# Kernel optimization log

Hardware: AMD Instinct MI355X
Metric: run time of the kernel (lower is better)

Reference implementation:

```python
import jax, jax.numpy as jnp
import numpy as np

B, CIN, COUT, H, W = 16, 128, 128, 64, 64
K1, K2, DIL = 3, 3, 1
PAD0 = DIL * (K1 - 1) // 2
PAD1 = DIL * (K2 - 1) // 2
L = H * W


def setup_inputs() -> dict:
    key = jax.random.key(0)
    k1, k2, k3, k4, k5 = jax.random.split(key, 5)
    x = jax.random.normal(k1, (B, CIN, H, W), dtype=jnp.float32)
    # binary per-pixel mask over kernel taps, broadcast over batch*channels
    mask = (jax.random.uniform(k2, (1, K1 * K2, L)) < 0.5).astype(jnp.float32)
    fan_in = CIN * K1 * K2
    bound = 1.0 / np.sqrt(fan_in)
    weight = jax.random.uniform(k3, (COUT, CIN, K1, K2), jnp.float32, -bound, bound)
    mask_weight = jax.random.uniform(k4, (COUT, K1, K2), jnp.float32, -bound, bound)
    bias = jax.random.uniform(k5, (COUT,), jnp.float32, -bound, bound)
    return {"x": x, "mask": mask, "weight": weight, "mask_weight": mask_weight, "bias": bias}


def reference(x, mask, weight, mask_weight, bias):
    # im2col: [B, CIN*K1*K2, H, W]; channel ordering (cin, k1, k2) matches torch unfold
    patches = jax.lax.conv_general_dilated_patches(
        x, (K1, K2), (1, 1), [(PAD0, PAD0), (PAD1, PAD1)], rhs_dilation=(DIL, DIL))
    p = patches.reshape(B, CIN, K1 * K2, L)
    p = p * mask[:, None, :, :]          # mask [1, K, L] broadcasts over B and CIN
    p = p.reshape(B, CIN * K1 * K2, L)
    out = jnp.einsum('ok,bkl->bol', weight.reshape(COUT, -1), p)
    out = out + bias[None, :, None]
    out = out + jnp.einsum('ok,mkl->mol', mask_weight.reshape(COUT, -1), mask)
    return out.reshape(B, COUT, H, W)
```

## Files before the change

### kernel.cpp

```cpp
#include <hip/hip_runtime.h>
#include <stdint.h>

#define B_    16
#define CIN_  128
#define COUT_ 128
#define H_    64
#define W_    64
#define L_    4096
#define KK_   1152
#define PW_   66
#define PPIX_ (PW_ * PW_)

typedef unsigned short u16;
typedef __bf16 bf16x8 __attribute__((ext_vector_type(8)));
typedef float  floatx4 __attribute__((ext_vector_type(4)));
typedef uint32_t u32x4 __attribute__((ext_vector_type(4)));

typedef const __attribute__((address_space(1))) uint32_t* gptr_t;
typedef __attribute__((address_space(3))) uint32_t*       lptr_t;

__device__ __forceinline__ void async_copy16(const void* g, void* l) {
    __builtin_amdgcn_global_load_lds((gptr_t)g, (lptr_t)l, 16, 0, 0);
}

__device__ __forceinline__ u16 f2bf(float f) {
    uint32_t u = __builtin_bit_cast(uint32_t, f);
    uint32_t r = u + 0x7FFFu + ((u >> 16) & 1u);
    return (u16)(r >> 16);
}

__global__ void lmc_transpose_kernel(const float* __restrict__ x, u16* __restrict__ xTp) {
    __shared__ u16 tile[64][CIN_ + 8];
    const int b   = blockIdx.y;
    const int y   = blockIdx.x;
    const int tid = threadIdx.x;

    {
        const int c  = tid >> 1;
        const int x0 = (tid & 1) * 32;
        const float* src = x + ((size_t)b * CIN_ + c) * L_ + y * 64 + x0;
        #pragma unroll
        for (int j = 0; j < 32; j += 4) {
            float4 v = *reinterpret_cast<const float4*>(src + j);
            tile[x0 + j + 0][c] = f2bf(v.x);
            tile[x0 + j + 1][c] = f2bf(v.y);
            tile[x0 + j + 2][c] = f2bf(v.z);
            tile[x0 + j + 3][c] = f2bf(v.w);
        }
    }
    __syncthreads();

    u16* dstrow = xTp + ((size_t)(b * PW_ + (y + 1)) * PW_) * CIN_;
    {
        const int xx   = tid >> 2;
        const int cseg = (tid & 3) * 32;
        u16* dst = dstrow + (size_t)(xx + 1) * CIN_ + cseg;
        #pragma unroll
        for (int i = 0; i < 32; i += 8) {
            *reinterpret_cast<uint4*>(dst + i) =
                *reinterpret_cast<const uint4*>(&tile[xx][cseg + i]);
        }
    }
    const uint4 z = {0u, 0u, 0u, 0u};
    if (tid < 32) {
        const int pix = (tid >> 4) ? 65 : 0;
        *reinterpret_cast<uint4*>(dstrow + (size_t)pix * CIN_ + (tid & 15) * 8) = z;
    }
    if (y == 0 || y == 63) {
        u16* brow = xTp + ((size_t)(b * PW_ + (y == 0 ? 0 : 65)) * PW_) * CIN_;
        for (int i = tid; i < (PW_ * CIN_) / 8; i += 256)
            reinterpret_cast<uint4*>(brow)[i] = z;
    }
}

__global__ void lmc_prep_kernel(const float* __restrict__ mask, const float* __restrict__ mw,
                                const float* __restrict__ bias, const float* __restrict__ w,
                                float* __restrict__ mb, u16* __restrict__ wb2) {
    const int bid = blockIdx.x, tid = threadIdx.x;
    if (bid < 128) {
        const int o = bid;
        float m[9];
        #pragma unroll
        for (int k = 0; k < 9; ++k) m[k] = mw[o * 9 + k];
        const float bs = bias[o];
        for (int l = tid; l < L_; l += 256) {
            float s = bs;
            #pragma unroll
            for (int k = 0; k < 9; ++k) s += m[k] * mask[k * L_ + l];
            mb[o * L_ + l] = s;
        }
    } else {
        const int base = (bid - 128) * 2304;
        #pragma unroll
        for (int i = 0; i < 9; ++i) {
            const int e = base + i * 256 + tid;
            const int k = e >> 14;
            const int rem = e & 16383;
            const int o = rem >> 7, c = rem & 127;
            wb2[e] = f2bf(w[(size_t)o * KK_ + c * 9 + k]);
        }
    }
}

__global__ __launch_bounds__(256, 2)
void lmc_gemm_kernel(const u16* __restrict__ xTp, const u16* __restrict__ wb2,
                     const float* __restrict__ mask, const float* __restrict__ mb,
                     float* __restrict__ out) {
    __shared__ u16 A_lds[128 * 128];
    __shared__ u16 B_lds[128 * 128];

    const int b    = blockIdx.y;
    const int l0   = blockIdx.x * 128;
    const int tid  = threadIdx.x;
    const int lane = tid & 63;
    const int wv   = tid >> 6;
    const int wm   = (wv >> 1) * 64;
    const int wn   = (wv & 1) * 64;
    const int lrow = lane & 15;
    const int quad = lane >> 4;

    uint32_t goffA[8];
    uint32_t goffB[8];
    #pragma unroll
    for (int s = 0; s < 8; ++s) {
        const int row = wv * 32 + s * 4 + (lane >> 4);
        const int cc  = (lane & 15) ^ (row & 7);
        goffA[s] = (uint32_t)(row * 256 + cc * 16);
        const int l  = l0 + row;
        const int yy = (l >> 6) + 1, xx = (l & 63) + 1;
        const int p  = (b * PW_ + yy) * PW_ + xx;
        goffB[s] = (uint32_t)(p * 256 + cc * 16);
    }

    uint64_t bits = 0;
    #pragma unroll
    for (int j = 0; j < 4; ++j) {
        const int l = l0 + wn + j * 16 + lrow;
        #pragma unroll
        for (int k = 0; k < 9; ++k)
            if (mask[k * L_ + l] != 0.0f) bits |= (1ull << (k * 4 + j));
    }

    floatx4 acc[4][4];
    #pragma unroll
    for (int i = 0; i < 4; ++i)
        #pragma unroll
        for (int j = 0; j < 4; ++j)
            acc[i][j] = (floatx4){0.f, 0.f, 0.f, 0.f};

    const char* xTp_c = (const char*)xTp;
    const char* wb2_c = (const char*)wb2;
    char* Ab = (char*)A_lds;
    char* Bb = (char*)B_lds;
    const int ldsbase = (wv * 8) * 1024;

    for (int k = 0; k < 9; ++k) {
        const int dy = k / 3 - 1;
        const int dx = k - (k / 3) * 3 - 1;
        const int tapoff = (dy * PW_ + dx) * 256;
        const int abase  = k * 32768;

        #pragma unroll
        for (int s = 0; s < 8; ++s)
            async_copy16(wb2_c + abase + goffA[s], Ab + ldsbase + s * 1024);
        #pragma unroll
        for (int s = 0; s < 8; ++s)
            async_copy16(xTp_c + (int)goffB[s] + tapoff, Bb + ldsbase + s * 1024);

        __syncthreads();

        uint32_t kp[4];
        #pragma unroll
        for (int j = 0; j < 4; ++j)
            kp[j] = 0u - (uint32_t)((bits >> (k * 4 + j)) & 1ull);

        #pragma unroll
        for (int ks = 0; ks < 4; ++ks) {
            const int sc = ((ks * 4 + quad) ^ (lrow & 7)) * 8;
            bf16x8 af[4], bfr[4];
            #pragma unroll
            for (int i = 0; i < 4; ++i)
                af[i] = *reinterpret_cast<const bf16x8*>(&A_lds[(wm + i * 16 + lrow) * 128 + sc]);
            #pragma unroll
            for (int j = 0; j < 4; ++j) {
                bf16x8 v = *reinterpret_cast<const bf16x8*>(&B_lds[(wn + j * 16 + lrow) * 128 + sc]);
                u32x4 t = __builtin_bit_cast(u32x4, v);
                t &= kp[j];
                bfr[j] = __builtin_bit_cast(bf16x8, t);
            }
            #pragma unroll
            for (int i = 0; i < 4; ++i)
                #pragma unroll
                for (int j = 0; j < 4; ++j)
                    acc[i][j] = __builtin_amdgcn_mfma_f32_16x16x32_bf16(af[i], bfr[j], acc[i][j], 0, 0, 0);
        }
        __syncthreads();
    }

    #pragma unroll
    for (int i = 0; i < 4; ++i) {
        #pragma unroll
        for (int j = 0; j < 4; ++j) {
            const int l = l0 + wn + j * 16 + lrow;
            #pragma unroll
            for (int r = 0; r < 4; ++r) {
                const int o = wm + i * 16 + quad * 4 + r;
                out[((size_t)b * COUT_ + o) * L_ + l] = acc[i][j][r] + mb[o * L_ + l];
            }
        }
    }
}

extern "C" void kernel_launch(void* const* d_in, const int* in_sizes, int n_in,
                              void* d_out, int out_size, void* d_ws, size_t ws_size,
                              hipStream_t stream) {
    const float* x      = (const float*)d_in[0];
    const float* mask   = (const float*)d_in[1];
    const float* weight = (const float*)d_in[2];
    const float* mw     = (const float*)d_in[3];
    const float* bias   = (const float*)d_in[4];
    float* out = (float*)d_out;

    char* ws = (char*)d_ws;
    u16*   xTp = (u16*)ws;
    u16*   wb2 = (u16*)(ws + 17842176);
    float* mb  = (float*)(ws + 17842176 + 294912);

    lmc_transpose_kernel<<<dim3(64, B_), 256, 0, stream>>>(x, xTp);
    lmc_prep_kernel<<<192, 256, 0, stream>>>(mask, mw, bias, weight, mb, wb2);
    lmc_gemm_kernel<<<dim3(L_ / 128, B_), 256, 0, stream>>>(xTp, wb2, mask, mb, out);
}
```

Measured before the change: 126.9 us.

## Load a 4-row input window once into LDS and read weights directly from global

The two prep kernels are merged into one launch, with an extra grid row handling the weight conversion and mask-bias precompute. The GEMM kernel now loads a 4-row padded input window (the tile's rows plus halo) into LDS once, and serves all nine taps from it with shifted column addresses. The per-tap barriers and LDS restaging go away. Weight fragments are read straight from global/L2 instead of LDS, and out-of-row taps are zeroed through the mask bits. This trades repeated LDS staging for uncached-layout global weight loads, which may add latency inside the MFMA loop.

```diff
diff --git a/kernel.cpp b/kernel.cpp
--- a/kernel.cpp
+++ b/kernel.cpp
@@ -9,7 +9,6 @@
 #define L_    4096
 #define KK_   1152
 #define PW_   66
-#define PPIX_ (PW_ * PW_)
 
 typedef unsigned short u16;
 typedef __bf16 bf16x8 __attribute__((ext_vector_type(8)));
@@ -29,12 +28,43 @@
     return (u16)(r >> 16);
 }
 
-__global__ void lmc_transpose_kernel(const float* __restrict__ x, u16* __restrict__ xTp) {
+__global__ void lmc_pre_kernel(const float* __restrict__ x, u16* __restrict__ xTp,
+                               const float* __restrict__ mask, const float* __restrict__ mw,
+                               const float* __restrict__ bias, const float* __restrict__ w,
+                               float* __restrict__ mb, u16* __restrict__ wb2) {
     __shared__ u16 tile[64][CIN_ + 8];
-    const int b   = blockIdx.y;
-    const int y   = blockIdx.x;
     const int tid = threadIdx.x;
 
+    if (blockIdx.y == 16) {
+        const int bid = blockIdx.x;
+        const int base = bid * 2304;
+        #pragma unroll
+        for (int i = 0; i < 9; ++i) {
+            const int e = base + i * 256 + tid;
+            const int k = e >> 14;
+            const int rem = e & 16383;
+            const int o = rem >> 7, c = rem & 127;
+            wb2[e] = f2bf(w[(size_t)o * KK_ + c * 9 + k]);
+        }
+        #pragma unroll
+        for (int oo = 0; oo < 2; ++oo) {
+            const int o = bid * 2 + oo;
+            float m[9];
+            #pragma unroll
+            for (int k = 0; k < 9; ++k) m[k] = mw[o * 9 + k];
+            const float bs = bias[o];
+            for (int l = tid; l < L_; l += 256) {
+                float s = bs;
+                #pragma unroll
+                for (int k = 0; k < 9; ++k) s += m[k] * mask[k * L_ + l];
+                mb[o * L_ + l] = s;
+            }
+        }
+        return;
+    }
+
+    const int b = blockIdx.y;
+    const int y = blockIdx.x;
     {
         const int c  = tid >> 1;
         const int x0 = (tid & 1) * 32;
@@ -73,44 +103,15 @@
     }
 }
 
-__global__ void lmc_prep_kernel(const float* __restrict__ mask, const float* __restrict__ mw,
-                                const float* __restrict__ bias, const float* __restrict__ w,
-                                float* __restrict__ mb, u16* __restrict__ wb2) {
-    const int bid = blockIdx.x, tid = threadIdx.x;
-    if (bid < 128) {
-        const int o = bid;
-        float m[9];
-        #pragma unroll
-        for (int k = 0; k < 9; ++k) m[k] = mw[o * 9 + k];
-        const float bs = bias[o];
-        for (int l = tid; l < L_; l += 256) {
-            float s = bs;
-            #pragma unroll
-            for (int k = 0; k < 9; ++k) s += m[k] * mask[k * L_ + l];
-            mb[o * L_ + l] = s;
-        }
-    } else {
-        const int base = (bid - 128) * 2304;
-        #pragma unroll
-        for (int i = 0; i < 9; ++i) {
-            const int e = base + i * 256 + tid;
-            const int k = e >> 14;
-            const int rem = e & 16383;
-            const int o = rem >> 7, c = rem & 127;
-            wb2[e] = f2bf(w[(size_t)o * KK_ + c * 9 + k]);
-        }
-    }
-}
-
 __global__ __launch_bounds__(256, 2)
 void lmc_gemm_kernel(const u16* __restrict__ xTp, const u16* __restrict__ wb2,
                      const float* __restrict__ mask, const float* __restrict__ mb,
                      float* __restrict__ out) {
-    __shared__ u16 A_lds[128 * 128];
-    __shared__ u16 B_lds[128 * 128];
+    __shared__ u16 Bwin[4 * 64 * 128];
 
     const int b    = blockIdx.y;
-    const int l0   = blockIdx.x * 128;
+    const int tile = blockIdx.x;
+    const int l0   = tile * 128;
     const int tid  = threadIdx.x;
     const int lane = tid & 63;
     const int wv   = tid >> 6;
@@ -119,26 +120,30 @@
     const int lrow = lane & 15;
     const int quad = lane >> 4;
 
-    uint32_t goffA[8];
-    uint32_t goffB[8];
-    #pragma unroll
-    for (int s = 0; s < 8; ++s) {
-        const int row = wv * 32 + s * 4 + (lane >> 4);
-        const int cc  = (lane & 15) ^ (row & 7);
-        goffA[s] = (uint32_t)(row * 256 + cc * 16);
-        const int l  = l0 + row;
-        const int yy = (l >> 6) + 1, xx = (l & 63) + 1;
-        const int p  = (b * PW_ + yy) * PW_ + xx;
-        goffB[s] = (uint32_t)(p * 256 + cc * 16);
+    {
+        const char* srcrow = (const char*)xTp
+            + ((size_t)((b * PW_) + tile * 2 + wv) * PW_ + 1) * 256;
+        char* dst = (char*)Bwin + wv * 16384;
+        const int cl = lane >> 4;
+        #pragma unroll
+        for (int seg = 0; seg < 16; ++seg) {
+            const int col = seg * 4 + cl;
+            const int ch  = (lane & 15) ^ (col & 7);
+            async_copy16(srcrow + col * 256 + ch * 16, dst + seg * 1024);
+        }
     }
 
     uint64_t bits = 0;
     #pragma unroll
     for (int j = 0; j < 4; ++j) {
-        const int l = l0 + wn + j * 16 + lrow;
-        #pragma unroll
-        for (int k = 0; k < 9; ++k)
-            if (mask[k * L_ + l] != 0.0f) bits |= (1ull << (k * 4 + j));
+        const int xl  = j * 16 + lrow;
+        const int l_g = l0 + wn + xl;
+        #pragma unroll
+        for (int k = 0; k < 9; ++k) {
+            const int dx = k - (k / 3) * 3 - 1;
+            const bool xok = (unsigned)(xl + dx) < 64u;
+            if (xok && mask[k * L_ + l_g] != 0.0f) bits |= (1ull << (k * 4 + j));
+        }
     }
 
     floatx4 acc[4][4];
@@ -148,27 +153,29 @@
         for (int j = 0; j < 4; ++j)
             acc[i][j] = (floatx4){0.f, 0.f, 0.f, 0.f};
 
-    const char* xTp_c = (const char*)xTp;
+    int rowA[4];
+    #pragma unroll
+    for (int i = 0; i < 4; ++i) rowA[i] = (wm + i * 16 + lrow) * 256 + quad * 16;
+    const int ywave = wn >> 6;
     const char* wb2_c = (const char*)wb2;
-    char* Ab = (char*)A_lds;
-    char* Bb = (char*)B_lds;
-    const int ldsbase = (wv * 8) * 1024;
+    const char* Bw = (const char*)Bwin;
+
+    __syncthreads();
 
     for (int k = 0; k < 9; ++k) {
         const int dy = k / 3 - 1;
         const int dx = k - (k / 3) * 3 - 1;
-        const int tapoff = (dy * PW_ + dx) * 256;
-        const int abase  = k * 32768;
-
-        #pragma unroll
-        for (int s = 0; s < 8; ++s)
-            async_copy16(wb2_c + abase + goffA[s], Ab + ldsbase + s * 1024);
-        #pragma unroll
-        for (int s = 0; s < 8; ++s)
-            async_copy16(xTp_c + (int)goffB[s] + tapoff, Bb + ldsbase + s * 1024);
-
-        __syncthreads();
-
+        const char* Ak = wb2_c + k * 32768;
+        const int rowbase = (ywave + 1 + dy) * 16384;
+
+        int baddr[4], c7[4];
+        #pragma unroll
+        for (int j = 0; j < 4; ++j) {
+            int col = j * 16 + lrow + dx;
+            col = min(max(col, 0), 63);
+            baddr[j] = rowbase + col * 256;
+            c7[j] = col & 7;
+        }
         uint32_t kp[4];
         #pragma unroll
         for (int j = 0; j < 4; ++j)
@@ -176,14 +183,14 @@
 
         #pragma unroll
         for (int ks = 0; ks < 4; ++ks) {
-            const int sc = ((ks * 4 + quad) ^ (lrow & 7)) * 8;
             bf16x8 af[4], bfr[4];
             #pragma unroll
             for (int i = 0; i < 4; ++i)
-                af[i] = *reinterpret_cast<const bf16x8*>(&A_lds[(wm + i * 16 + lrow) * 128 + sc]);
+                af[i] = *reinterpret_cast<const bf16x8*>(Ak + rowA[i] + ks * 64);
             #pragma unroll
             for (int j = 0; j < 4; ++j) {
-                bf16x8 v = *reinterpret_cast<const bf16x8*>(&B_lds[(wn + j * 16 + lrow) * 128 + sc]);
+                const int slot = ((ks * 4 + quad) ^ c7[j]) * 16;
+                bf16x8 v = *reinterpret_cast<const bf16x8*>(Bw + baddr[j] + slot);
                 u32x4 t = __builtin_bit_cast(u32x4, v);
                 t &= kp[j];
                 bfr[j] = __builtin_bit_cast(bf16x8, t);
@@ -194,7 +201,6 @@
                 for (int j = 0; j < 4; ++j)
                     acc[i][j] = __builtin_amdgcn_mfma_f32_16x16x32_bf16(af[i], bfr[j], acc[i][j], 0, 0, 0);
         }
-        __syncthreads();
     }
 
     #pragma unroll
@@ -226,7 +232,6 @@
     u16*   wb2 = (u16*)(ws + 17842176);
     float* mb  = (float*)(ws + 17842176 + 294912);
 
-    lmc_transpose_kernel<<<dim3(64, B_), 256, 0, stream>>>(x, xTp);
-    lmc_prep_kernel<<<192, 256, 0, stream>>>(mask, mw, bias, weight, mb, wb2);
-    lmc_gemm_kernel<<<dim3(L_ / 128, B_), 256, 0, stream>>>(xTp, wb2, mask, mb, out);
-}
+    lmc_pre_kernel<<<dim3(64, 17), 256, 0, stream>>>(x, xTp, mask, mw, bias, weight, mb, wb2);
+    lmc_gemm_kernel<<<dim3(32, 16), 256, 0, stream>>>(xTp, wb2, mask, mb, out);
+}
```

New measurement: 145.1 us. 14.3% more time.
